# Optimization experiments

Measured on AMD Instinct MI355X. Metric: run time of the kernel, lower is better.

The kernel has to match this reference:

```python
import jax, jax.numpy as jnp
import numpy as np

N, E, R, B, H, C = 50000, 1600000, 50, 30, 16, 4


def setup_inputs() -> dict:
    key = jax.random.key(0)
    ks = jax.random.split(key, 12)
    edge_index = jax.random.randint(ks[0], (2, E), 0, N, dtype=jnp.int64)
    edge_type = jax.random.randint(ks[1], (E,), 0, R, dtype=jnp.int64)
    edge_norm = jax.random.uniform(ks[2], (E,), dtype=jnp.float32)
    s = 0.1
    basis1 = jax.random.normal(ks[3], (B, N, H), dtype=jnp.float32) * s
    comp1 = jax.random.normal(ks[4], (R, B), dtype=jnp.float32) * s
    root1 = jax.random.normal(ks[5], (N, H), dtype=jnp.float32) * s
    bias1 = jnp.zeros((H,), dtype=jnp.float32)
    basis2 = jax.random.normal(ks[6], (B, H, C), dtype=jnp.float32) * s
    comp2 = jax.random.normal(ks[7], (R, B), dtype=jnp.float32) * s
    root2 = jax.random.normal(ks[8], (H, C), dtype=jnp.float32) * s
    bias2 = jnp.zeros((C,), dtype=jnp.float32)
    return {
        "edge_index": edge_index, "edge_type": edge_type, "edge_norm": edge_norm,
        "basis1": basis1, "comp1": comp1, "root1": root1, "bias1": bias1,
        "basis2": basis2, "comp2": comp2, "root2": root2, "bias2": bias2,
    }


def _scatter_mean(msg, dst, n):
    # mean aggregation over destination nodes (PyG RGCNConv aggr='mean')
    summed = jnp.zeros((n, msg.shape[1]), dtype=msg.dtype).at[dst].add(msg)
    cnt = jnp.zeros((n,), dtype=msg.dtype).at[dst].add(1.0)
    return summed / jnp.maximum(cnt, 1.0)[:, None]


def reference(edge_index, edge_type, edge_norm, basis1, comp1, root1, bias1,
              basis2, comp2, root2, bias2):
    # edge_norm is accepted but unused, matching the original forward
    src, dst = edge_index[0], edge_index[1]
    n = root1.shape[0]
    # ---- layer 1: x is None -> per-(relation, src-node) weight row lookup ----
    w1 = jnp.einsum('rb,bnh->rnh', comp1, basis1)       # [R, N, H]
    msg1 = w1[edge_type, src]                           # [E, H] gather
    x = _scatter_mean(msg1, dst, n) + root1 + bias1      # root added directly (x=None)
    x = jax.nn.relu(x)
    # ---- layer 2: standard basis-decomposed RGCN on dense features ----
    w2 = jnp.einsum('rb,bhc->rhc', comp2, basis2)       # [R, H, C]
    msg2 = jnp.einsum('eh,ehc->ec', x[src], w2[edge_type])  # per-edge transform
    out = _scatter_mean(msg2, dst, n) + x @ root2 + bias2
    return jax.nn.log_softmax(out, axis=1)
```

## Files before the change

kernel.cpp:

```cpp
#include <hip/hip_runtime.h>
#include <math.h>

#define N_NODES 50000
#define E_EDGES 1600000
#define R_REL   50
#define B_BAS   30
#define H_DIM   16
#define C_DIM   4
#define NH      (N_NODES * H_DIM)

__global__ __launch_bounds__(256) void k_w1(const float* __restrict__ basis1,
                                            const float* __restrict__ comp1,
                                            float* __restrict__ w1) {
    __shared__ float s_comp[R_REL * B_BAS];
    for (int i = threadIdx.x; i < R_REL * B_BAS; i += blockDim.x)
        s_comp[i] = comp1[i];
    __syncthreads();

    const int idx = blockIdx.x * blockDim.x + threadIdx.x;
    if (idx >= NH) return;

    float bv[B_BAS];
#pragma unroll
    for (int b = 0; b < B_BAS; ++b) bv[b] = basis1[b * NH + idx];

    for (int r = 0; r < R_REL; ++r) {
        float acc = 0.f;
#pragma unroll
        for (int b = 0; b < B_BAS; ++b) acc += s_comp[r * B_BAS + b] * bv[b];
        w1[(size_t)r * NH + idx] = acc;
    }
}

__global__ __launch_bounds__(256) void k_w2(const float* __restrict__ basis2,
                                            const float* __restrict__ comp2,
                                            float* __restrict__ w2) {
    const int HC = H_DIM * C_DIM;
    for (int idx = threadIdx.x; idx < R_REL * HC; idx += blockDim.x) {
        int r = idx / HC;
        int hc = idx % HC;
        float acc = 0.f;
#pragma unroll
        for (int b = 0; b < B_BAS; ++b)
            acc += comp2[r * B_BAS + b] * basis2[b * HC + hc];
        w2[idx] = acc;
    }
}

__global__ __launch_bounds__(256) void k_hist(const int* __restrict__ ei,
                                              int* __restrict__ cnt_i) {
    const int e = blockIdx.x * blockDim.x + threadIdx.x;
    if (e < E_EDGES) atomicAdd(&cnt_i[ei[E_EDGES + e]], 1);
}

__global__ __launch_bounds__(256) void k_scan_part(const int* __restrict__ cnt_i,
                                                   int* __restrict__ part,
                                                   int* __restrict__ bsum) {
    const int i = blockIdx.x * 256 + threadIdx.x;
    const int lane = threadIdx.x & 63;
    const int wid = threadIdx.x >> 6;
    const int v = (i < N_NODES) ? cnt_i[i] : 0;
    int s = v;
#pragma unroll
    for (int d = 1; d < 64; d <<= 1) {
        int t = __shfl_up(s, d, 64);
        if (lane >= d) s += t;
    }
    __shared__ int wsum[4];
    if (lane == 63) wsum[wid] = s;
    __syncthreads();
    int woff = 0;
    for (int w = 0; w < wid; ++w) woff += wsum[w];
    if (i < N_NODES) part[i] = s - v + woff;
    if (threadIdx.x == 255) bsum[blockIdx.x] = woff + s;
}

__global__ __launch_bounds__(256) void k_scan_tops(const int* __restrict__ bsum,
                                                   int* __restrict__ boff) {
    const int NB = (N_NODES + 255) / 256;
    const int lane = threadIdx.x & 63;
    const int wid = threadIdx.x >> 6;
    const int v = (threadIdx.x < NB) ? bsum[threadIdx.x] : 0;
    int s = v;
#pragma unroll
    for (int d = 1; d < 64; d <<= 1) {
        int t = __shfl_up(s, d, 64);
        if (lane >= d) s += t;
    }
    __shared__ int wsum[4];
    if (lane == 63) wsum[wid] = s;
    __syncthreads();
    int woff = 0;
    for (int w = 0; w < wid; ++w) woff += wsum[w];
    if (threadIdx.x < NB) boff[threadIdx.x] = s - v + woff;
}

__global__ __launch_bounds__(256) void k_scan_add(const int* __restrict__ part,
                                                  const int* __restrict__ boff,
                                                  int* __restrict__ off,
                                                  int* __restrict__ cursor) {
    const int i = blockIdx.x * 256 + threadIdx.x;
    if (i < N_NODES) {
        const int o = part[i] + boff[blockIdx.x];
        off[i] = o;
        cursor[i] = o;
    }
    if (i == 0) off[N_NODES] = E_EDGES;
}

__global__ __launch_bounds__(256) void k_bucket(const int* __restrict__ ei,
                                                const int* __restrict__ et,
                                                int* __restrict__ cursor,
                                                unsigned* __restrict__ rec) {
    const int e = blockIdx.x * blockDim.x + threadIdx.x;
    if (e >= E_EDGES) return;
    const int src = ei[e];
    const int dst = ei[E_EDGES + e];
    const int r = et[e];
    const int pos = atomicAdd(&cursor[dst], 1);
    rec[pos] = (unsigned)src | ((unsigned)r << 16);
}

__global__ __launch_bounds__(256) void k_agg1x(const unsigned* __restrict__ rec,
                                               const int* __restrict__ off,
                                               const float* __restrict__ w1,
                                               const float* __restrict__ root1,
                                               const float* __restrict__ bias1,
                                               float* __restrict__ x) {
    const int wid = threadIdx.x >> 6;
    const int lane = threadIdx.x & 63;
    const int dst = blockIdx.x * 4 + wid;
    const int h = lane & 15;
    const int sub = lane >> 4;
    const int e0 = off[dst], e1 = off[dst + 1];

    float acc = 0.f;
    for (int e = e0 + sub; e < e1; e += 4) {
        const unsigned p = rec[e];
        const int src = (int)(p & 0xFFFFu);
        const int r = (int)(p >> 16);
        acc += w1[(size_t)r * NH + src * H_DIM + h];
    }
    acc += __shfl_xor(acc, 16, 64);
    acc += __shfl_xor(acc, 32, 64);

    if (sub == 0) {
        const float c = fmaxf((float)(e1 - e0), 1.f);
        const float v = acc / c + root1[dst * H_DIM + h] + bias1[h];
        x[dst * H_DIM + h] = fmaxf(v, 0.f);
    }
}

__global__ __launch_bounds__(256) void k_agg2out(const unsigned* __restrict__ rec,
                                                 const int* __restrict__ off,
                                                 const float* __restrict__ x,
                                                 const float* __restrict__ w2,
                                                 const float* __restrict__ root2,
                                                 const float* __restrict__ bias2,
                                                 float* __restrict__ out) {
    const int wid = threadIdx.x >> 6;
    const int lane = threadIdx.x & 63;
    const int dst = blockIdx.x * 4 + wid;
    const int h = lane & 15;
    const int sub = lane >> 4;
    const int e0 = off[dst], e1 = off[dst + 1];

    float a0 = 0.f, a1 = 0.f, a2 = 0.f, a3 = 0.f;
    for (int e = e0 + sub; e < e1; e += 4) {
        const unsigned p = rec[e];
        const int src = (int)(p & 0xFFFFu);
        const int r = (int)(p >> 16);
        const float xv = x[src * H_DIM + h];
        const float4 w = *(const float4*)(w2 + r * (H_DIM * C_DIM) + h * C_DIM);
        a0 += xv * w.x; a1 += xv * w.y; a2 += xv * w.z; a3 += xv * w.w;
    }
#pragma unroll
    for (int d = 1; d < 64; d <<= 1) {
        a0 += __shfl_xor(a0, d, 64);
        a1 += __shfl_xor(a1, d, 64);
        a2 += __shfl_xor(a2, d, 64);
        a3 += __shfl_xor(a3, d, 64);
    }

    if (lane == 0) {
        const float c = fmaxf((float)(e1 - e0), 1.f);
        float y0 = a0 / c + bias2[0];
        float y1 = a1 / c + bias2[1];
        float y2 = a2 / c + bias2[2];
        float y3 = a3 / c + bias2[3];
#pragma unroll
        for (int hh = 0; hh < H_DIM; ++hh) {
            const float xv = x[dst * H_DIM + hh];
            const float4 w = *(const float4*)(root2 + hh * C_DIM);
            y0 += xv * w.x; y1 += xv * w.y; y2 += xv * w.z; y3 += xv * w.w;
        }
        const float m = fmaxf(fmaxf(y0, y1), fmaxf(y2, y3));
        const float s = expf(y0 - m) + expf(y1 - m) + expf(y2 - m) + expf(y3 - m);
        const float lse = m + logf(s);
        out[dst * 4 + 0] = y0 - lse;
        out[dst * 4 + 1] = y1 - lse;
        out[dst * 4 + 2] = y2 - lse;
        out[dst * 4 + 3] = y3 - lse;
    }
}

extern "C" void kernel_launch(void* const* d_in, const int* in_sizes, int n_in,
                              void* d_out, int out_size, void* d_ws, size_t ws_size,
                              hipStream_t stream) {
    const int*   edge_index = (const int*)d_in[0];
    const int*   edge_type  = (const int*)d_in[1];
    const float* basis1 = (const float*)d_in[3];
    const float* comp1  = (const float*)d_in[4];
    const float* root1  = (const float*)d_in[5];
    const float* bias1  = (const float*)d_in[6];
    const float* basis2 = (const float*)d_in[7];
    const float* comp2  = (const float*)d_in[8];
    const float* root2  = (const float*)d_in[9];
    const float* bias2  = (const float*)d_in[10];

    float* out = (float*)d_out;

    char* ws = (char*)d_ws;
    size_t o = 0;
    auto take = [&](size_t bytes) { char* p = ws + o; o += (bytes + 15) & ~(size_t)15; return p; };

    float*    w1     = (float*)   take((size_t)R_REL * NH * sizeof(float));
    unsigned* rec    = (unsigned*)take((size_t)E_EDGES * sizeof(unsigned));
    float*    x      = (float*)   take((size_t)NH * sizeof(float));
    int*      part   = (int*)x;
    int*      off    = (int*)     take((size_t)(N_NODES + 1) * sizeof(int));
    int*      cnt_i  = (int*)     take((size_t)N_NODES * sizeof(int));
    int*      cursor = (int*)     take((size_t)N_NODES * sizeof(int));
    float*    w2     = (float*)   take((size_t)R_REL * H_DIM * C_DIM * sizeof(float));
    int*      bsum   = (int*)     take(256 * sizeof(int));
    int*      boff   = (int*)     take(256 * sizeof(int));
    (void)ws_size;

    const int NB = (N_NODES + 255) / 256;

    hipMemsetAsync(cnt_i, 0, (size_t)N_NODES * sizeof(int), stream);

    k_w1<<<(NH + 255) / 256, 256, 0, stream>>>(basis1, comp1, w1);
    k_w2<<<1, 256, 0, stream>>>(basis2, comp2, w2);

    k_hist<<<(E_EDGES + 255) / 256, 256, 0, stream>>>(edge_index, cnt_i);
    k_scan_part<<<NB, 256, 0, stream>>>(cnt_i, part, bsum);
    k_scan_tops<<<1, 256, 0, stream>>>(bsum, boff);
    k_scan_add<<<NB, 256, 0, stream>>>(part, boff, off, cursor);
    k_bucket<<<(E_EDGES + 255) / 256, 256, 0, stream>>>(edge_index, edge_type, cursor, rec);

    k_agg1x<<<N_NODES / 4, 256, 0, stream>>>(rec, off, w1, root1, bias1, x);

    k_agg2out<<<N_NODES / 4, 256, 0, stream>>>(rec, off, x, w2, root2, bias2, out);
}
```

Measured before the change: 514.2 us.

## Merge w1/w2/histogram kernels and slice bucket scatter by destination range

Fuses the w1 basis expansion, w2 expansion and degree histogram into one launch, so the independent phases can run at the same time and two launches go away. The bucket kernel now launches 8 blocks per edge chunk. Each block keeps only edges whose destination falls in its node slice, so concurrent atomics and record writes stay inside a narrower address range and scatter locality should improve. In exchange, every edge's destination index is read 8 times and most threads exit early, which adds load traffic and wasted threads.

```diff
diff --git a/kernel.cpp b/kernel.cpp
--- a/kernel.cpp
+++ b/kernel.cpp
@@ -9,48 +9,52 @@
 #define C_DIM   4
 #define NH      (N_NODES * H_DIM)
 
-__global__ __launch_bounds__(256) void k_w1(const float* __restrict__ basis1,
-                                            const float* __restrict__ comp1,
-                                            float* __restrict__ w1) {
-    __shared__ float s_comp[R_REL * B_BAS];
-    for (int i = threadIdx.x; i < R_REL * B_BAS; i += blockDim.x)
-        s_comp[i] = comp1[i];
-    __syncthreads();
-
-    const int idx = blockIdx.x * blockDim.x + threadIdx.x;
-    if (idx >= NH) return;
-
-    float bv[B_BAS];
-#pragma unroll
-    for (int b = 0; b < B_BAS; ++b) bv[b] = basis1[b * NH + idx];
-
-    for (int r = 0; r < R_REL; ++r) {
-        float acc = 0.f;
-#pragma unroll
-        for (int b = 0; b < B_BAS; ++b) acc += s_comp[r * B_BAS + b] * bv[b];
-        w1[(size_t)r * NH + idx] = acc;
-    }
-}
-
-__global__ __launch_bounds__(256) void k_w2(const float* __restrict__ basis2,
-                                            const float* __restrict__ comp2,
-                                            float* __restrict__ w2) {
-    const int HC = H_DIM * C_DIM;
-    for (int idx = threadIdx.x; idx < R_REL * HC; idx += blockDim.x) {
-        int r = idx / HC;
-        int hc = idx % HC;
-        float acc = 0.f;
-#pragma unroll
-        for (int b = 0; b < B_BAS; ++b)
-            acc += comp2[r * B_BAS + b] * basis2[b * HC + hc];
-        w2[idx] = acc;
-    }
-}
-
-__global__ __launch_bounds__(256) void k_hist(const int* __restrict__ ei,
-                                              int* __restrict__ cnt_i) {
-    const int e = blockIdx.x * blockDim.x + threadIdx.x;
-    if (e < E_EDGES) atomicAdd(&cnt_i[ei[E_EDGES + e]], 1);
+#define NSLICE      8
+#define SLICE_NODES (N_NODES / NSLICE)
+
+#define W1_BLOCKS   (NH / 256)
+#define HIST_BLOCKS (E_EDGES / 256)
+
+__global__ __launch_bounds__(256) void k_front(const float* __restrict__ basis1,
+                                               const float* __restrict__ comp1,
+                                               float* __restrict__ w1,
+                                               const float* __restrict__ basis2,
+                                               const float* __restrict__ comp2,
+                                               float* __restrict__ w2,
+                                               const int* __restrict__ ei,
+                                               int* __restrict__ cnt_i) {
+    if (blockIdx.x < W1_BLOCKS) {
+        __shared__ float s_comp[R_REL * B_BAS];
+        for (int i = threadIdx.x; i < R_REL * B_BAS; i += 256)
+            s_comp[i] = comp1[i];
+        __syncthreads();
+
+        const int idx = blockIdx.x * 256 + threadIdx.x;
+        float bv[B_BAS];
+#pragma unroll
+        for (int b = 0; b < B_BAS; ++b) bv[b] = basis1[b * NH + idx];
+
+        for (int r = 0; r < R_REL; ++r) {
+            float acc = 0.f;
+#pragma unroll
+            for (int b = 0; b < B_BAS; ++b) acc += s_comp[r * B_BAS + b] * bv[b];
+            w1[(size_t)r * NH + idx] = acc;
+        }
+    } else if (blockIdx.x < W1_BLOCKS + HIST_BLOCKS) {
+        const int e = (blockIdx.x - W1_BLOCKS) * 256 + threadIdx.x;
+        atomicAdd(&cnt_i[ei[E_EDGES + e]], 1);
+    } else {
+        const int HC = H_DIM * C_DIM;
+        for (int idx = threadIdx.x; idx < R_REL * HC; idx += 256) {
+            const int r = idx / HC;
+            const int hc = idx % HC;
+            float acc = 0.f;
+#pragma unroll
+            for (int b = 0; b < B_BAS; ++b)
+                acc += comp2[r * B_BAS + b] * basis2[b * HC + hc];
+            w2[idx] = acc;
+        }
+    }
 }
 
 __global__ __launch_bounds__(256) void k_scan_part(const int* __restrict__ cnt_i,
@@ -112,10 +116,16 @@
                                                 const int* __restrict__ et,
                                                 int* __restrict__ cursor,
                                                 unsigned* __restrict__ rec) {
-    const int e = blockIdx.x * blockDim.x + threadIdx.x;
+    const int chunk = blockIdx.x >> 3;
+    const int slice = blockIdx.x & (NSLICE - 1);
+    const int lo = slice * SLICE_NODES;
+
+    const int e = chunk * 256 + threadIdx.x;
     if (e >= E_EDGES) return;
+    const int dst = ei[E_EDGES + e];
+    if ((unsigned)(dst - lo) >= (unsigned)SLICE_NODES) return;
+
     const int src = ei[e];
-    const int dst = ei[E_EDGES + e];
     const int r = et[e];
     const int pos = atomicAdd(&cursor[dst], 1);
     rec[pos] = (unsigned)src | ((unsigned)r << 16);
@@ -240,14 +250,16 @@
 
     hipMemsetAsync(cnt_i, 0, (size_t)N_NODES * sizeof(int), stream);
 
-    k_w1<<<(NH + 255) / 256, 256, 0, stream>>>(basis1, comp1, w1);
-    k_w2<<<1, 256, 0, stream>>>(basis2, comp2, w2);
-
-    k_hist<<<(E_EDGES + 255) / 256, 256, 0, stream>>>(edge_index, cnt_i);
+    k_front<<<W1_BLOCKS + HIST_BLOCKS + 1, 256, 0, stream>>>(
+        basis1, comp1, w1, basis2, comp2, w2, edge_index, cnt_i);
+
     k_scan_part<<<NB, 256, 0, stream>>>(cnt_i, part, bsum);
     k_scan_tops<<<1, 256, 0, stream>>>(bsum, boff);
     k_scan_add<<<NB, 256, 0, stream>>>(part, boff, off, cursor);
-    k_bucket<<<(E_EDGES + 255) / 256, 256, 0, stream>>>(edge_index, edge_type, cursor, rec);
+    {
+        const int chunks = (E_EDGES + 255) / 256;
+        k_bucket<<<chunks * NSLICE, 256, 0, stream>>>(edge_index, edge_type, cursor, rec);
+    }
 
     k_agg1x<<<N_NODES / 4, 256, 0, stream>>>(rec, off, w1, root1, bias1, x);
 
```

Measured after the change: 451.4 us. 1.14x faster.
